# Kernel tuning notes

Hardware: AMD Instinct MI355X
Metric: run time of the kernel (lower is better)

Reference implementation:

```python
import jax, jax.numpy as jnp
import numpy as np

NUM_BINS = 20
EMBED_DIM = 768
NUM_CODES = 1000
BATCH = 131072
EPS = 1e-8


def setup_inputs() -> dict:
    key = jax.random.key(0)
    k1, k2, k3, k4 = jax.random.split(key, 4)
    values = jax.random.uniform(k1, (BATCH,), dtype=jnp.float32)
    code_ids = jax.random.randint(k2, (BATCH,), 0, NUM_CODES, dtype=jnp.int32)
    # per-code sorted quantile boundaries, shape (NUM_CODES, NUM_BINS-1)
    boundaries = jnp.sort(
        jax.random.uniform(k3, (NUM_CODES, NUM_BINS - 1), dtype=jnp.float32), axis=1
    )
    embed_table = jax.random.normal(k4, (NUM_BINS, EMBED_DIM), dtype=jnp.float32)
    return {
        "values": values,
        "code_ids": code_ids,
        "boundaries": boundaries,
        "embed_table": embed_table,
    }


def reference(values, code_ids, boundaries, embed_table):
    nb = embed_table.shape[0]  # num_bins
    # gather each sample's boundary row: (B, nb-1)
    brows = boundaries[code_ids]
    # torch.searchsorted default == side='left'
    idx = jax.vmap(jnp.searchsorted)(brows, values)
    idx = jnp.clip(idx, 0, nb - 1)
    interior = (idx > 0) & (idx < nb - 1)
    # boundary gathers (clipped so edge rows stay in range; masked out below)
    lo_b = jnp.take_along_axis(brows, jnp.clip(idx - 1, 0, nb - 2)[:, None], axis=1)[:, 0]
    hi_b = jnp.take_along_axis(brows, jnp.clip(idx, 0, nb - 2)[:, None], axis=1)[:, 0]
    denom = hi_b - lo_b
    tiny = jnp.abs(denom) < EPS
    safe_denom = jnp.where(tiny, 1.0, denom)
    alpha = jnp.where(tiny, 0.5, jnp.clip((values - lo_b) / safe_denom, 0.0, 1.0))
    # at edge bins the original returns a single bin embedding (alpha irrelevant)
    alpha = jnp.where(interior, alpha, 0.0)
    lower_idx = jnp.where(idx == 0, 0, jnp.where(idx >= nb - 1, nb - 1, idx - 1))
    upper_idx = jnp.where(interior, idx, lower_idx)
    a = alpha[:, None]
    out = (1.0 - a) * embed_table[lower_idx] + a * embed_table[upper_idx]
    return out  # (B, EMBED_DIM)
```

## Files before the change

kernel.cpp:

```cpp
#include <hip/hip_runtime.h>
#include <cfloat>

#define NB      20
#define NBOUND  19
#define ED      768
#define ED4     192
#define EPS     1e-8f

__global__ __launch_bounds__(256) void sde_kernel(
    const float* __restrict__ values,
    const int*   __restrict__ code_ids,
    const float* __restrict__ boundaries,
    const float* __restrict__ embed_table,
    float*       __restrict__ out,
    int batch)
{
    const int wave = blockIdx.x * (blockDim.x >> 6) + (threadIdx.x >> 6);
    const int lane = threadIdx.x & 63;
    if (wave >= batch) return;
    const int b = wave;

    const float v = values[b];
    const int   c = code_ids[b];

    float bnd = FLT_MAX;
    if (lane < NBOUND) bnd = boundaries[(size_t)c * NBOUND + lane];

    const unsigned long long lt = __ballot(bnd < v);
    const int idx = __popcll(lt);

    int lo_i = idx - 1; lo_i = lo_i < 0 ? 0 : lo_i;
    int hi_i = idx > NBOUND - 1 ? NBOUND - 1 : idx;
    const float lo_b = __shfl(bnd, lo_i);
    const float hi_b = __shfl(bnd, hi_i);

    const bool interior = (idx > 0) && (idx < NB - 1);
    const float denom = hi_b - lo_b;
    const bool tiny = fabsf(denom) < EPS;

    float alpha = (v - lo_b) / (tiny ? 1.0f : denom);
    alpha = fminf(fmaxf(alpha, 0.0f), 1.0f);
    if (tiny)      alpha = 0.5f;
    if (!interior) alpha = 0.0f;

    const int lower = (idx == 0) ? 0 : ((idx >= NB - 1) ? NB - 1 : idx - 1);
    const int upper = interior ? idx : lower;

    const float4* __restrict__ tlo = (const float4*)(embed_table + (size_t)lower * ED);
    const float4* __restrict__ thi = (const float4*)(embed_table + (size_t)upper * ED);
    float4* __restrict__ orow = (float4*)(out + (size_t)b * ED);

    const float om = 1.0f - alpha;
    #pragma unroll
    for (int k = 0; k < 3; ++k) {
        const int s = lane + k * 64;
        const float4 e0 = tlo[s];
        const float4 e1 = thi[s];
        float4 r;
        r.x = om * e0.x + alpha * e1.x;
        r.y = om * e0.y + alpha * e1.y;
        r.z = om * e0.z + alpha * e1.z;
        r.w = om * e0.w + alpha * e1.w;
        orow[s] = r;
    }
}

extern "C" void kernel_launch(void* const* d_in, const int* in_sizes, int n_in,
                              void* d_out, int out_size, void* d_ws, size_t ws_size,
                              hipStream_t stream)
{
    const float* values     = (const float*)d_in[0];
    const int*   code_ids   = (const int*)  d_in[1];
    const float* boundaries = (const float*)d_in[2];
    const float* embed      = (const float*)d_in[3];
    float*       out        = (float*)d_out;

    const int batch = in_sizes[0];
    const int waves_per_block = 4;
    const int blocks = (batch + waves_per_block - 1) / waves_per_block;

    sde_kernel<<<blocks, 256, 0, stream>>>(values, code_ids, boundaries, embed, out, batch);
}
```

Baseline: 405.6 us.

## Compute bin/alpha per row in one thread, then wave-stream 128 rows per block

The kernel now splits into two phases. First, each of 128 threads computes the bucket index and alpha for one row with a scalar linear scan over its 19 boundaries and stores the results in shared memory. After a block barrier, each of the four waves loops over 32 rows and writes the interpolated 768-float embedding rows. This replaces the per-row wave ballot/shuffle search and the one-row-per-wave launch with far fewer blocks that each do more output work. The cost is half the threads idling during the search phase and a __syncthreads per block.

```diff
diff --git a/kernel.cpp b/kernel.cpp
--- a/kernel.cpp
+++ b/kernel.cpp
@@ -1,11 +1,10 @@
 #include <hip/hip_runtime.h>
-#include <cfloat>
 
 #define NB      20
 #define NBOUND  19
 #define ED      768
-#define ED4     192
 #define EPS     1e-8f
+#define RPB     128
 
 __global__ __launch_bounds__(256) void sde_kernel(
     const float* __restrict__ values,
@@ -15,53 +14,77 @@
     float*       __restrict__ out,
     int batch)
 {
-    const int wave = blockIdx.x * (blockDim.x >> 6) + (threadIdx.x >> 6);
-    const int lane = threadIdx.x & 63;
-    if (wave >= batch) return;
-    const int b = wave;
+    __shared__ float s_alpha[RPB];
+    __shared__ int   s_lo[RPB];
+    __shared__ int   s_hi[RPB];
 
-    const float v = values[b];
-    const int   c = code_ids[b];
+    const int tid  = threadIdx.x;
+    const int base = blockIdx.x * RPB;
 
-    float bnd = FLT_MAX;
-    if (lane < NBOUND) bnd = boundaries[(size_t)c * NBOUND + lane];
+    if (tid < RPB && base + tid < batch) {
+        const int b = base + tid;
+        const float v = values[b];
+        const int   c = code_ids[b];
+        const float* __restrict__ br = boundaries + (size_t)c * NBOUND;
 
-    const unsigned long long lt = __ballot(bnd < v);
-    const int idx = __popcll(lt);
+        float bb[NBOUND];
+        #pragma unroll
+        for (int j = 0; j < NBOUND; ++j) bb[j] = br[j];
 
-    int lo_i = idx - 1; lo_i = lo_i < 0 ? 0 : lo_i;
-    int hi_i = idx > NBOUND - 1 ? NBOUND - 1 : idx;
-    const float lo_b = __shfl(bnd, lo_i);
-    const float hi_b = __shfl(bnd, hi_i);
+        int idx = 0;
+        #pragma unroll
+        for (int j = 0; j < NBOUND; ++j) idx += (bb[j] < v) ? 1 : 0;
 
-    const bool interior = (idx > 0) && (idx < NB - 1);
-    const float denom = hi_b - lo_b;
-    const bool tiny = fabsf(denom) < EPS;
+        float lo_b = bb[0];
+        #pragma unroll
+        for (int j = 1; j < NBOUND; ++j) if (bb[j] < v) lo_b = bb[j];
 
-    float alpha = (v - lo_b) / (tiny ? 1.0f : denom);
-    alpha = fminf(fmaxf(alpha, 0.0f), 1.0f);
-    if (tiny)      alpha = 0.5f;
-    if (!interior) alpha = 0.0f;
+        float hi_b = bb[NBOUND - 1];
+        #pragma unroll
+        for (int j = NBOUND - 2; j >= 0; --j) if (bb[j] >= v) hi_b = bb[j];
 
-    const int lower = (idx == 0) ? 0 : ((idx >= NB - 1) ? NB - 1 : idx - 1);
-    const int upper = interior ? idx : lower;
+        const bool interior = (idx > 0) && (idx < NB - 1);
+        const float denom = hi_b - lo_b;
+        const bool tiny = fabsf(denom) < EPS;
 
-    const float4* __restrict__ tlo = (const float4*)(embed_table + (size_t)lower * ED);
-    const float4* __restrict__ thi = (const float4*)(embed_table + (size_t)upper * ED);
-    float4* __restrict__ orow = (float4*)(out + (size_t)b * ED);
+        float alpha = (v - lo_b) / (tiny ? 1.0f : denom);
+        alpha = fminf(fmaxf(alpha, 0.0f), 1.0f);
+        if (tiny)      alpha = 0.5f;
+        if (!interior) alpha = 0.0f;
 
-    const float om = 1.0f - alpha;
-    #pragma unroll
-    for (int k = 0; k < 3; ++k) {
-        const int s = lane + k * 64;
-        const float4 e0 = tlo[s];
-        const float4 e1 = thi[s];
-        float4 r;
-        r.x = om * e0.x + alpha * e1.x;
-        r.y = om * e0.y + alpha * e1.y;
-        r.z = om * e0.z + alpha * e1.z;
-        r.w = om * e0.w + alpha * e1.w;
-        orow[s] = r;
+        const int lower = (idx == 0) ? 0 : ((idx >= NB - 1) ? NB - 1 : idx - 1);
+        const int upper = interior ? idx : lower;
+
+        s_alpha[tid] = alpha;
+        s_lo[tid]    = lower * ED;
+        s_hi[tid]    = upper * ED;
+    }
+    __syncthreads();
+
+    const int wave = tid >> 6;
+    const int lane = tid & 63;
+
+    const int rows = (batch - base < RPB) ? (batch - base) : RPB;
+    #pragma unroll 2
+    for (int r = wave; r < rows; r += 4) {
+        const float a  = s_alpha[r];
+        const float om = 1.0f - a;
+        const float4* __restrict__ tlo = (const float4*)(embed_table + s_lo[r]);
+        const float4* __restrict__ thi = (const float4*)(embed_table + s_hi[r]);
+        float4* __restrict__ orow = (float4*)(out + (size_t)(base + r) * ED) + lane;
+
+        #pragma unroll
+        for (int k = 0; k < 3; ++k) {
+            const int s = lane + k * 64;
+            const float4 e0 = tlo[s];
+            const float4 e1 = thi[s];
+            float4 o;
+            o.x = om * e0.x + a * e1.x;
+            o.y = om * e0.y + a * e1.y;
+            o.z = om * e0.z + a * e1.z;
+            o.w = om * e0.w + a * e1.w;
+            orow[k * 64] = o;
+        }
     }
 }
 
@@ -75,9 +98,8 @@
     const float* embed      = (const float*)d_in[3];
     float*       out        = (float*)d_out;
 
-    const int batch = in_sizes[0];
-    const int waves_per_block = 4;
-    const int blocks = (batch + waves_per_block - 1) / waves_per_block;
+    const int batch  = in_sizes[0];
+    const int blocks = (batch + RPB - 1) / RPB;
 
     sde_kernel<<<blocks, 256, 0, stream>>>(values, code_ids, boundaries, embed, out, batch);
 }
```

Result: slower. 471.4 us (+16.2%).
